# Kernel tuning notes

Measured on AMD Instinct MI355X. Metric: run time of the kernel, lower is better.

The kernel has to match this reference:

```python
import jax, jax.numpy as jnp
import numpy as np

N = 65536      # num ref nodes
M = 65536      # num query nodes
E = 1572864    # num edges (avg degree 24)
K0 = 27        # num kernels (3x3x3 neighborhood)
D1 = 64        # input channels
D2 = 64        # output channels


def setup_inputs() -> dict:
    key = jax.random.key(0)
    k1, k2, k3, k4, k5, k6 = jax.random.split(key, 6)
    # kernel init mirrors initialize_kernel_weight (uniform in [-bound, bound])
    fan_in = D1 * K0
    gain = float(np.sqrt(2.0 / (1.0 + 5.0)))  # leaky_relu gain with slope sqrt(5)
    std = gain / np.sqrt(fan_in)
    bound = float(np.sqrt(3.0) * std)
    kernel = jax.random.uniform(k1, (K0, D1, D2), minval=-bound, maxval=bound, dtype=jnp.float32)
    ref_feat = jax.random.normal(k2, (N, D1), dtype=jnp.float32)
    e_kernel = jax.random.randint(k3, (E,), 0, K0)
    e_ref = jax.random.randint(k4, (E,), 0, N)
    e_query = jax.random.randint(k5, (E,), 0, M)
    e_weight = jax.random.uniform(k6, (E,), dtype=jnp.float32)
    return {
        "kernel": kernel,
        "ref_feat": ref_feat,
        "e_kernel": e_kernel,
        "e_ref": e_ref,
        "e_query": e_query,
        "num_queries": M,
        "e_weight": e_weight,
    }


def reference(kernel, ref_feat, e_kernel, e_ref, e_query, num_queries, e_weight):
    # Math of MessagePassing.forward:
    #   query_feat[m] = sum_{edges e: e_query[e]==m} w_e * (ref_feat[e_ref[e]] @ kernel[e_kernel[e]])
    # Efficient form: precompute each node's transform under every kernel
    # (N*K0*D1*D2 dense GEMM), then gather per edge and scatter-reduce.
    transformed = jnp.einsum('nd,kdo->nko', ref_feat, kernel)   # [N, K0, D2]
    msgs = transformed[e_ref, e_kernel] * e_weight[:, None]      # [E, D2]
    query_feat = jax.ops.segment_sum(msgs, e_query, num_segments=num_queries)  # [M, D2]
    return query_feat
```

## Files before the change

### kernel.cpp

```cpp
#include <hip/hip_runtime.h>

#define DIN 64
#define DOUT 64
#define MAXK 32

typedef __bf16 bf16x8 __attribute__((ext_vector_type(8)));
typedef float  f32x4  __attribute__((ext_vector_type(4)));
typedef unsigned int u32x4 __attribute__((ext_vector_type(4)));

static __device__ inline unsigned short f2b(float x) {
    return __builtin_bit_cast(unsigned short, (__bf16)x);
}
static __device__ inline float b2f(unsigned short u) {
    return __uint_as_float(((unsigned int)u) << 16);
}


__global__ void conv_w_kernel(const float* __restrict__ W,
                              unsigned short* __restrict__ Wt, int total,
                              int* __restrict__ qcount) {
    int i = blockIdx.x * blockDim.x + threadIdx.x;
    if (i < 256) qcount[i] = 0;
    if (i < total) {
        int j    = i & 7;
        int lane = (i >> 3) & 63;
        int h    = (i >> 9) & 1;
        int t    = (i >> 10) & 3;
        int k    = i >> 12;
        int col  = lane & 15;
        int quad = lane >> 4;
        int d1 = h * 32 + quad * 8 + j;
        int d2 = t * 16 + col;
        Wt[i] = f2b(W[(k * 64 + d1) * 64 + d2]);
    }
}


static __device__ __forceinline__ void phaseA_body(
    const float* __restrict__ ref,
    const unsigned short* __restrict__ Wt,
    unsigned short* __restrict__ T,
    int K0, int Nn, int nblk, char* lds)
{
    const int lane = threadIdx.x & 63;
    const int wid  = threadIdx.x >> 6;
    const int col  = lane & 15;
    const int quad = lane >> 4;
    const int n0   = nblk * 64 + wid * 16;
    const int row  = n0 + col;
    char* buf = lds + wid * (16 * 144);

    const float* rp = ref + (size_t)row * 64;
    f32x4 r0 = *reinterpret_cast<const f32x4*>(rp + quad * 8);
    f32x4 r1 = *reinterpret_cast<const f32x4*>(rp + quad * 8 + 4);
    f32x4 r2 = *reinterpret_cast<const f32x4*>(rp + 32 + quad * 8);
    f32x4 r3 = *reinterpret_cast<const f32x4*>(rp + 32 + quad * 8 + 4);
    bf16x8 b0, b1;
    #pragma unroll
    for (int i = 0; i < 4; ++i) {
        b0[i]     = (__bf16)r0[i];
        b0[4 + i] = (__bf16)r1[i];
        b1[i]     = (__bf16)r2[i];
        b1[4 + i] = (__bf16)r3[i];
    }

    const int rrow = lane >> 2;
    const int rq   = lane & 3;

    for (int k = 0; k < K0; ++k) {
        const unsigned short* Wk = Wt + (size_t)k * 4096;
        #pragma unroll
        for (int t = 0; t < 4; ++t) {
            const unsigned short* ap = Wk + (size_t)t * 1024 + lane * 8;
            bf16x8 a0 = *reinterpret_cast<const bf16x8*>(ap);
            bf16x8 a1 = *reinterpret_cast<const bf16x8*>(ap + 512);
            f32x4 c = {0.f, 0.f, 0.f, 0.f};
            c = __builtin_amdgcn_mfma_f32_16x16x32_bf16(a0, b0, c, 0, 0, 0);
            c = __builtin_amdgcn_mfma_f32_16x16x32_bf16(a1, b1, c, 0, 0, 0);
            unsigned int lo = (unsigned int)f2b(c[0]) | ((unsigned int)f2b(c[1]) << 16);
            unsigned int hi = (unsigned int)f2b(c[2]) | ((unsigned int)f2b(c[3]) << 16);
            *reinterpret_cast<uint2*>(buf + col * 144 + t * 32 + quad * 8) =
                make_uint2(lo, hi);
        }
        u32x4 v0 = *reinterpret_cast<const u32x4*>(buf + rrow * 144 + rq * 32);
        u32x4 v1 = *reinterpret_cast<const u32x4*>(buf + rrow * 144 + rq * 32 + 16);
        size_t gbase = ((size_t)k * Nn + n0 + rrow) * 64 + rq * 16;
        *reinterpret_cast<u32x4*>(T + gbase)     = v0;
        *reinterpret_cast<u32x4*>(T + gbase + 8) = v1;
    }
}


__global__ void p1_hist_kernel(const int* __restrict__ eq, int E,
                               int* __restrict__ qcount) {
    __shared__ int l[256];
    l[threadIdx.x] = 0;
    __syncthreads();
    int stride = gridDim.x * blockDim.x;
    for (int i = blockIdx.x * blockDim.x + threadIdx.x; i < E; i += stride)
        atomicAdd(&l[((unsigned)eq[i]) >> 8], 1);
    __syncthreads();
    int v = l[threadIdx.x];
    if (v) atomicAdd(&qcount[threadIdx.x], v);
}

__global__ void p1_scan_kernel(const int* __restrict__ qcount,
                               int* __restrict__ gbase, int* __restrict__ gcursor,
                               int* __restrict__ qstart, int NB, int M, int E) {
    __shared__ int sh[256];
    int t = threadIdx.x;
    int v = (t < NB) ? qcount[t] : 0;
    sh[t] = v;
    __syncthreads();
    #pragma unroll
    for (int o = 1; o < 256; o <<= 1) {
        int x = (t >= o) ? sh[t - o] : 0;
        __syncthreads();
        sh[t] += x;
        __syncthreads();
    }
    int ex = sh[t] - v;
    if (t < NB) { gbase[t] = ex; gcursor[t] = ex; }
    if (t == 0) qstart[M] = E;
}

static __device__ __forceinline__ void scatter_body(
    const int* __restrict__ eq, const int* __restrict__ er,
    const int* __restrict__ ek, const float* __restrict__ ew,
    int E, int* __restrict__ gcursor, uint2* __restrict__ tmp,
    int sblk, int* bin, int* base)
{
    const int t = threadIdx.x;
    bin[t] = 0;
    __syncthreads();
    const int i0 = sblk * 4096;
    unsigned key[16];
    unsigned rank[16];
    uint2 pay[16];
    #pragma unroll
    for (int u = 0; u < 16; ++u) {
        int i = i0 + u * 256 + t;
        if (i < E) {
            int q = eq[i];
            unsigned b = ((unsigned)q) >> 8;
            key[u] = b;
            rank[u] = atomicAdd(&bin[b], 1);
            pay[u] = make_uint2((unsigned)er[i] | ((unsigned)ek[i] << 16) |
                                ((unsigned)(q & 255) << 21),
                                __float_as_uint(ew[i]));
        } else {
            key[u] = 0xFFFFFFFFu;
        }
    }
    __syncthreads();
    int c = bin[t];
    if (c) base[t] = atomicAdd(&gcursor[t], c);
    __syncthreads();
    #pragma unroll
    for (int u = 0; u < 16; ++u) {
        if (key[u] != 0xFFFFFFFFu)
            tmp[(size_t)base[key[u]] + rank[u]] = pay[u];
    }
}

static __device__ __forceinline__ void p2_body(
    const uint2* __restrict__ tmp, const int* __restrict__ gbase,
    const int* __restrict__ qcount, uint2* __restrict__ rec,
    int* __restrict__ qstart, int b, int* fine, int* foff)
{
    const int t = threadIdx.x;
    const int s = gbase[b];
    const int L = qcount[b];
    fine[t] = 0;
    __syncthreads();
    for (int i = t; i < L; i += 256)
        atomicAdd(&fine[(tmp[s + i].x >> 21) & 255], 1);
    __syncthreads();
    int v = fine[t];
    __syncthreads();
    #pragma unroll
    for (int o = 1; o < 256; o <<= 1) {
        int x = (t >= o) ? fine[t - o] : 0;
        __syncthreads();
        fine[t] += x;
        __syncthreads();
    }
    foff[t] = fine[t] - v;
    qstart[b * 256 + t] = s + foff[t];
    __syncthreads();
    fine[t] = 0;
    __syncthreads();
    for (int i = t; i < L; i += 256) {
        uint2 p = tmp[s + i];
        unsigned fb = (p.x >> 21) & 255;
        int r = atomicAdd(&fine[fb], 1);
        rec[(size_t)s + foff[fb] + r] = p;
    }
}


__global__ __launch_bounds__(256) void fusedA_scatter_kernel(
    const float* __restrict__ ref, const unsigned short* __restrict__ Wt,
    unsigned short* __restrict__ T, int K0, int Nn, int NA1,
    const int* __restrict__ eq, const int* __restrict__ er,
    const int* __restrict__ ek, const float* __restrict__ ew,
    int E, int* __restrict__ gcursor, uint2* __restrict__ tmp)
{
    __shared__ __align__(16) char ldsbuf[4 * 16 * 144];
    __shared__ int s0[256];
    __shared__ int s1[256];
    if ((int)blockIdx.x < NA1) {
        phaseA_body(ref, Wt, T, K0, Nn, (int)blockIdx.x, ldsbuf);
    } else {
        scatter_body(eq, er, ek, ew, E, gcursor, tmp,
                     (int)blockIdx.x - NA1, s0, s1);
    }
}

__global__ __launch_bounds__(256) void fusedA_p2_kernel(
    const float* __restrict__ ref, const unsigned short* __restrict__ Wt,
    unsigned short* __restrict__ T, int K0, int Nn, int NA1, int NA2,
    const uint2* __restrict__ tmp, const int* __restrict__ gbase,
    const int* __restrict__ qcount, uint2* __restrict__ rec,
    int* __restrict__ qstart)
{
    __shared__ __align__(16) char ldsbuf[4 * 16 * 144];
    __shared__ int s0[256];
    __shared__ int s1[256];
    if ((int)blockIdx.x < NA2) {
        phaseA_body(ref, Wt, T, K0, Nn, NA1 + (int)blockIdx.x, ldsbuf);
    } else {
        p2_body(tmp, gbase, qcount, rec, qstart,
                (int)blockIdx.x - NA2, s0, s1);
    }
}


__global__ __launch_bounds__(256) void phaseB_kernel(
    const unsigned short* __restrict__ T,
    const uint2* __restrict__ rec,
    const int* __restrict__ qstart,
    float* __restrict__ out, int Nn)
{
    const int lane = threadIdx.x & 63;
    const int wid  = threadIdx.x >> 6;
    const int q    = blockIdx.x * 4 + wid;

    int beg = qstart[q];
    int end = qstart[q + 1];
    int cnt = end - beg;
    float acc = 0.f;

    if (cnt <= 64) {
        uint2 rv = make_uint2(0u, 0u);
        if (lane < cnt) rv = rec[beg + lane];
        int j = 0;
        for (; j + 8 <= cnt; j += 8) {
            float partial[8];
            #pragma unroll
            for (int u = 0; u < 8; ++u) {
                unsigned mx = (unsigned)__builtin_amdgcn_readlane((int)rv.x, j + u);
                unsigned mw = (unsigned)__builtin_amdgcn_readlane((int)rv.y, j + u);
                unsigned off = (((mx >> 16) & 31) * (unsigned)Nn + (mx & 0xFFFFu)) * 64u
                               + (unsigned)lane;
                partial[u] = __uint_as_float(mw) * b2f(T[off]);
            }
            #pragma unroll
            for (int u = 0; u < 8; ++u) acc += partial[u];
        }
        for (; j < cnt; ++j) {
            unsigned mx = (unsigned)__builtin_amdgcn_readlane((int)rv.x, j);
            unsigned mw = (unsigned)__builtin_amdgcn_readlane((int)rv.y, j);
            unsigned off = (((mx >> 16) & 31) * (unsigned)Nn + (mx & 0xFFFFu)) * 64u
                           + (unsigned)lane;
            acc = fmaf(__uint_as_float(mw), b2f(T[off]), acc);
        }
    } else {
        for (int j = beg; j < end; ++j) {
            uint2 v0 = rec[j];
            unsigned m0 = __builtin_amdgcn_readfirstlane(v0.x);
            float w0 = __uint_as_float(__builtin_amdgcn_readfirstlane(v0.y));
            unsigned off = (((m0 >> 16) & 31) * (unsigned)Nn + (m0 & 0xFFFFu)) * 64u
                           + (unsigned)lane;
            acc = fmaf(w0, b2f(T[off]), acc);
        }
    }
    out[(size_t)q * 64 + lane] = acc;
}


__global__ void hist_kernel(const int* __restrict__ ek, int E, int* __restrict__ counts) {
    __shared__ int l[MAXK];
    if (threadIdx.x < MAXK) l[threadIdx.x] = 0;
    __syncthreads();
    int stride = gridDim.x * blockDim.x;
    for (int i = blockIdx.x * blockDim.x + threadIdx.x; i < E; i += stride)
        atomicAdd(&l[ek[i]], 1);
    __syncthreads();
    if (threadIdx.x < MAXK) {
        int v = l[threadIdx.x];
        if (v) atomicAdd(&counts[threadIdx.x], v);
    }
}

__global__ void scan_kernel(const int* __restrict__ counts, int K,
                            int* __restrict__ start, int* __restrict__ cursor) {
    if (threadIdx.x == 0 && blockIdx.x == 0) {
        int acc = 0;
        for (int k = 0; k < K; ++k) {
            start[k] = acc;
            cursor[k] = acc;
            acc += counts[k];
        }
    }
}

__global__ void scatter_kernel(const int* __restrict__ ek, int E,
                               int* __restrict__ cursor, int* __restrict__ sorted) {
    __shared__ int lcnt[MAXK], lbase[MAXK], lpos[MAXK];
    if (threadIdx.x < MAXK) { lcnt[threadIdx.x] = 0; lpos[threadIdx.x] = 0; }
    __syncthreads();
    int i = blockIdx.x * blockDim.x + threadIdx.x;
    int k = 0;
    bool valid = (i < E);
    if (valid) { k = ek[i]; atomicAdd(&lcnt[k], 1); }
    __syncthreads();
    if (threadIdx.x < MAXK) {
        int v = lcnt[threadIdx.x];
        if (v) lbase[threadIdx.x] = atomicAdd(&cursor[threadIdx.x], v);
    }
    __syncthreads();
    if (valid) {
        int slot = lbase[k] + atomicAdd(&lpos[k], 1);
        sorted[slot] = i;
    }
}

__global__ __launch_bounds__(256) void mp_bucket_kernel(
    const float* __restrict__ W, const float* __restrict__ ref,
    const int* __restrict__ e_ref, const int* __restrict__ e_query,
    const float* __restrict__ e_weight, const int* __restrict__ sorted,
    const int* __restrict__ start, const int* __restrict__ counts,
    float* __restrict__ out)
{
    const int k = blockIdx.y;
    const int lane = threadIdx.x & 63;
    const int wid = threadIdx.x >> 6;

    float wreg[DIN];
    const float* Wk = W + k * DIN * DOUT;
    #pragma unroll
    for (int d = 0; d < DIN; ++d) wreg[d] = Wk[d * DOUT + lane];

    const int s = start[k];
    const int c = counts[k];
    const int nwaves = gridDim.x * 4;

    for (int i = blockIdx.x * 4 + wid; i < c; i += nwaves) {
        int eid = __builtin_amdgcn_readfirstlane(sorted[s + i]);
        int r = e_ref[eid];
        int q = e_query[eid];
        float w = e_weight[eid];
        const float* row = ref + r * DIN;
        float a0 = 0.f, a1 = 0.f, a2 = 0.f, a3 = 0.f;
        #pragma unroll
        for (int d = 0; d < DIN; d += 4) {
            a0 += row[d + 0] * wreg[d + 0];
            a1 += row[d + 1] * wreg[d + 1];
            a2 += row[d + 2] * wreg[d + 2];
            a3 += row[d + 3] * wreg[d + 3];
        }
        atomicAdd(&out[q * DOUT + lane], ((a0 + a1) + (a2 + a3)) * w);
    }
}


extern "C" void kernel_launch(void* const* d_in, const int* in_sizes, int n_in,
                              void* d_out, int out_size, void* d_ws, size_t ws_size,
                              hipStream_t stream) {
    const float* W        = (const float*)d_in[0];
    const float* ref      = (const float*)d_in[1];
    const int*   e_kernel = (const int*)d_in[2];
    const int*   e_ref    = (const int*)d_in[3];
    const int*   e_query  = (const int*)d_in[4];
    const float* e_weight = (const float*)d_in[6];

    const int K0 = in_sizes[0] / (DIN * DOUT);
    const int N  = in_sizes[1] / DIN;
    const int E  = in_sizes[2];
    const int M  = out_size / DOUT;
    const int KD = K0 * 64;
    const int NB = M / 256;

    float* out = (float*)d_out;

    size_t off = 0;
    auto alloc = [&](size_t bytes, size_t align) {
        off = (off + align - 1) / align * align;
        size_t r = off; off += bytes; return r;
    };
    size_t o_tmp     = alloc((size_t)E * 8, 16);
    size_t o_rec     = alloc((size_t)E * 8, 16);
    size_t o_qstart  = alloc((size_t)(M + 1) * 4, 4);
    size_t o_qcount  = alloc(256 * 4, 4);
    size_t o_gbase   = alloc(256 * 4, 4);
    size_t o_gcursor = alloc(256 * 4, 4);
    size_t o_wt      = alloc((size_t)K0 * 4096 * 2, 16);
    size_t o_T       = alloc((size_t)N * KD * 2, 16);
    size_t needA = off;

    bool planA_ok = (ws_size >= needA) && (M % 256 == 0) && (NB >= 1) && (NB <= 256) &&
                    (N % 64 == 0) && (N <= 65536) && (K0 <= 32);

    if (planA_ok) {
        char* ws = (char*)d_ws;
        uint2* tmp           = (uint2*)(ws + o_tmp);
        uint2* rec           = (uint2*)(ws + o_rec);
        int*  qstart         = (int*)(ws + o_qstart);
        int*  qcount         = (int*)(ws + o_qcount);
        int*  gbase          = (int*)(ws + o_gbase);
        int*  gcursor        = (int*)(ws + o_gcursor);
        unsigned short* Wt   = (unsigned short*)(ws + o_wt);
        unsigned short* T    = (unsigned short*)(ws + o_T);

        const int NA  = N / 64;
        const int NA1 = (NA + 1) / 2;
        const int NA2 = NA - NA1;
        const int SCB = (E + 4095) / 4096;

        conv_w_kernel<<<(K0 * 4096 + 255) / 256, 256, 0, stream>>>(W, Wt, K0 * 4096,
                                                                   qcount);
        p1_hist_kernel<<<512, 256, 0, stream>>>(e_query, E, qcount);
        p1_scan_kernel<<<1, 256, 0, stream>>>(qcount, gbase, gcursor, qstart, NB, M, E);

        fusedA_scatter_kernel<<<NA1 + SCB, 256, 0, stream>>>(
            ref, Wt, T, K0, N, NA1,
            e_query, e_ref, e_kernel, e_weight, E, gcursor, tmp);

        fusedA_p2_kernel<<<NA2 + NB, 256, 0, stream>>>(
            ref, Wt, T, K0, N, NA1, NA2,
            tmp, gbase, qcount, rec, qstart);

        phaseB_kernel<<<M / 4, 256, 0, stream>>>(T, rec, qstart, out, N);
    } else {
        hipMemsetAsync(out, 0, (size_t)out_size * sizeof(float), stream);
        size_t needB = (size_t)(96 + E) * sizeof(int);
        if (ws_size >= needB) {
            int* ws_i   = (int*)d_ws;
            int* counts = ws_i;
            int* start  = ws_i + 32;
            int* cursor = ws_i + 64;
            int* sorted = ws_i + 96;
            hipMemsetAsync(counts, 0, 96 * sizeof(int), stream);
            hist_kernel<<<512, 256, 0, stream>>>(e_kernel, E, counts);
            scan_kernel<<<1, 64, 0, stream>>>(counts, K0, start, cursor);
            scatter_kernel<<<(E + 255) / 256, 256, 0, stream>>>(e_kernel, E, cursor, sorted);
            dim3 grid(64, K0);
            mp_bucket_kernel<<<grid, 256, 0, stream>>>(W, ref, e_ref, e_query, e_weight,
                                                       sorted, start, counts, out);
        }
    }
}
```

Before: 269.6 us.

## Split phase-A GEMM across four fused launches and prefetch weights in registers

The dense node-by-kernel transform (phase A) is now split into four unevenly sized chunks. Each chunk is co-launched with one of the CSR-build stages (histogram, scan, scatter, fine sort), so the lightweight sort stages overlap with GEMM work instead of running alone. Inside phase A, the next kernel slice's weight fragments are prefetched into registers and the LDS staging buffer is double-buffered by k parity. The larger LDS allocation and extra prefetch registers may reduce occupancy.

After: 276.0 us. +2.4%, slower.

```diff
diff --git a/kernel.cpp b/kernel.cpp
--- a/kernel.cpp
+++ b/kernel.cpp
@@ -36,6 +36,8 @@
 }
 
 
+#define PA_LDS 18432
+
 static __device__ __forceinline__ void phaseA_body(
     const float* __restrict__ ref,
     const unsigned short* __restrict__ Wt,
@@ -48,7 +50,7 @@
     const int quad = lane >> 4;
     const int n0   = nblk * 64 + wid * 16;
     const int row  = n0 + col;
-    char* buf = lds + wid * (16 * 144);
+    char* bufs = lds + wid * 4608;
 
     const float* rp = ref + (size_t)row * 64;
     f32x4 r0 = *reinterpret_cast<const f32x4*>(rp + quad * 8);
@@ -66,48 +68,77 @@
 
     const int rrow = lane >> 2;
     const int rq   = lane & 3;
+    const unsigned short* Wl = Wt + lane * 8;
+
+    bf16x8 c0 = *reinterpret_cast<const bf16x8*>(Wl);
+    bf16x8 c1 = *reinterpret_cast<const bf16x8*>(Wl + 512);
+    bf16x8 c2 = *reinterpret_cast<const bf16x8*>(Wl + 1024);
+    bf16x8 c3 = *reinterpret_cast<const bf16x8*>(Wl + 1536);
+    bf16x8 c4 = *reinterpret_cast<const bf16x8*>(Wl + 2048);
+    bf16x8 c5 = *reinterpret_cast<const bf16x8*>(Wl + 2560);
+    bf16x8 c6 = *reinterpret_cast<const bf16x8*>(Wl + 3072);
+    bf16x8 c7 = *reinterpret_cast<const bf16x8*>(Wl + 3584);
 
     for (int k = 0; k < K0; ++k) {
-        const unsigned short* Wk = Wt + (size_t)k * 4096;
-        #pragma unroll
-        for (int t = 0; t < 4; ++t) {
-            const unsigned short* ap = Wk + (size_t)t * 1024 + lane * 8;
-            bf16x8 a0 = *reinterpret_cast<const bf16x8*>(ap);
-            bf16x8 a1 = *reinterpret_cast<const bf16x8*>(ap + 512);
-            f32x4 c = {0.f, 0.f, 0.f, 0.f};
-            c = __builtin_amdgcn_mfma_f32_16x16x32_bf16(a0, b0, c, 0, 0, 0);
-            c = __builtin_amdgcn_mfma_f32_16x16x32_bf16(a1, b1, c, 0, 0, 0);
-            unsigned int lo = (unsigned int)f2b(c[0]) | ((unsigned int)f2b(c[1]) << 16);
-            unsigned int hi = (unsigned int)f2b(c[2]) | ((unsigned int)f2b(c[3]) << 16);
-            *reinterpret_cast<uint2*>(buf + col * 144 + t * 32 + quad * 8) =
-                make_uint2(lo, hi);
+        bf16x8 p0, p1, p2, p3, p4, p5, p6, p7;
+        if (k + 1 < K0) {
+            const unsigned short* Wn = Wl + (size_t)(k + 1) * 4096;
+            p0 = *reinterpret_cast<const bf16x8*>(Wn);
+            p1 = *reinterpret_cast<const bf16x8*>(Wn + 512);
+            p2 = *reinterpret_cast<const bf16x8*>(Wn + 1024);
+            p3 = *reinterpret_cast<const bf16x8*>(Wn + 1536);
+            p4 = *reinterpret_cast<const bf16x8*>(Wn + 2048);
+            p5 = *reinterpret_cast<const bf16x8*>(Wn + 2560);
+            p6 = *reinterpret_cast<const bf16x8*>(Wn + 3072);
+            p7 = *reinterpret_cast<const bf16x8*>(Wn + 3584);
+        } else {
+            p0 = c0; p1 = c1; p2 = c2; p3 = c3;
+            p4 = c4; p5 = c5; p6 = c6; p7 = c7;
+        }
+        char* buf = bufs + (k & 1) * 2304;
+        {
+            f32x4 a;
+            a = (f32x4){0.f, 0.f, 0.f, 0.f};
+            a = __builtin_amdgcn_mfma_f32_16x16x32_bf16(c0, b0, a, 0, 0, 0);
+            a = __builtin_amdgcn_mfma_f32_16x16x32_bf16(c1, b1, a, 0, 0, 0);
+            *reinterpret_cast<uint2*>(buf + col * 144 + 0 * 32 + quad * 8) =
+                make_uint2((unsigned)f2b(a[0]) | ((unsigned)f2b(a[1]) << 16),
+                           (unsigned)f2b(a[2]) | ((unsigned)f2b(a[3]) << 16));
+            a = (f32x4){0.f, 0.f, 0.f, 0.f};
+            a = __builtin_amdgcn_mfma_f32_16x16x32_bf16(c2, b0, a, 0, 0, 0);
+            a = __builtin_amdgcn_mfma_f32_16x16x32_bf16(c3, b1, a, 0, 0, 0);
+            *reinterpret_cast<uint2*>(buf + col * 144 + 1 * 32 + quad * 8) =
+                make_uint2((unsigned)f2b(a[0]) | ((unsigned)f2b(a[1]) << 16),
+                           (unsigned)f2b(a[2]) | ((unsigned)f2b(a[3]) << 16));
+            a = (f32x4){0.f, 0.f, 0.f, 0.f};
+            a = __builtin_amdgcn_mfma_f32_16x16x32_bf16(c4, b0, a, 0, 0, 0);
+            a = __builtin_amdgcn_mfma_f32_16x16x32_bf16(c5, b1, a, 0, 0, 0);
+            *reinterpret_cast<uint2*>(buf + col * 144 + 2 * 32 + quad * 8) =
+                make_uint2((unsigned)f2b(a[0]) | ((unsigned)f2b(a[1]) << 16),
+                           (unsigned)f2b(a[2]) | ((unsigned)f2b(a[3]) << 16));
+            a = (f32x4){0.f, 0.f, 0.f, 0.f};
+            a = __builtin_amdgcn_mfma_f32_16x16x32_bf16(c6, b0, a, 0, 0, 0);
+            a = __builtin_amdgcn_mfma_f32_16x16x32_bf16(c7, b1, a, 0, 0, 0);
+            *reinterpret_cast<uint2*>(buf + col * 144 + 3 * 32 + quad * 8) =
+                make_uint2((unsigned)f2b(a[0]) | ((unsigned)f2b(a[1]) << 16),
+                           (unsigned)f2b(a[2]) | ((unsigned)f2b(a[3]) << 16));
         }
         u32x4 v0 = *reinterpret_cast<const u32x4*>(buf + rrow * 144 + rq * 32);
         u32x4 v1 = *reinterpret_cast<const u32x4*>(buf + rrow * 144 + rq * 32 + 16);
         size_t gbase = ((size_t)k * Nn + n0 + rrow) * 64 + rq * 16;
         *reinterpret_cast<u32x4*>(T + gbase)     = v0;
         *reinterpret_cast<u32x4*>(T + gbase + 8) = v1;
-    }
-}
-
-
-__global__ void p1_hist_kernel(const int* __restrict__ eq, int E,
-                               int* __restrict__ qcount) {
-    __shared__ int l[256];
-    l[threadIdx.x] = 0;
-    __syncthreads();
-    int stride = gridDim.x * blockDim.x;
-    for (int i = blockIdx.x * blockDim.x + threadIdx.x; i < E; i += stride)
-        atomicAdd(&l[((unsigned)eq[i]) >> 8], 1);
-    __syncthreads();
-    int v = l[threadIdx.x];
-    if (v) atomicAdd(&qcount[threadIdx.x], v);
-}
-
-__global__ void p1_scan_kernel(const int* __restrict__ qcount,
-                               int* __restrict__ gbase, int* __restrict__ gcursor,
-                               int* __restrict__ qstart, int NB, int M, int E) {
-    __shared__ int sh[256];
+        c0 = p0; c1 = p1; c2 = p2; c3 = p3;
+        c4 = p4; c5 = p5; c6 = p6; c7 = p7;
+    }
+}
+
+
+static __device__ __forceinline__ void scan_body(
+    const int* __restrict__ qcount, int* __restrict__ gbase,
+    int* __restrict__ gcursor, int* __restrict__ qstart,
+    int NB, int M, int E, int* sh)
+{
     int t = threadIdx.x;
     int v = (t < NB) ? qcount[t] : 0;
     sh[t] = v;
@@ -199,39 +230,77 @@
 }
 
 
+__global__ __launch_bounds__(256) void fusedA_hist_kernel(
+    const float* __restrict__ ref, const unsigned short* __restrict__ Wt,
+    unsigned short* __restrict__ T, int K0, int Nn, int acnt,
+    const int* __restrict__ eq, int E, int* __restrict__ qcount)
+{
+    __shared__ __align__(16) char ldsbuf[PA_LDS];
+    __shared__ int l[256];
+    if ((int)blockIdx.x < acnt) {
+        phaseA_body(ref, Wt, T, K0, Nn, (int)blockIdx.x, ldsbuf);
+    } else {
+        l[threadIdx.x] = 0;
+        __syncthreads();
+        const int nh = (int)gridDim.x - acnt;
+        const int stride = nh * 256;
+        for (int i = ((int)blockIdx.x - acnt) * 256 + (int)threadIdx.x; i < E;
+             i += stride)
+            atomicAdd(&l[((unsigned)eq[i]) >> 8], 1);
+        __syncthreads();
+        int v = l[threadIdx.x];
+        if (v) atomicAdd(&qcount[threadIdx.x], v);
+    }
+}
+
+__global__ __launch_bounds__(256) void fusedA_scan_kernel(
+    const float* __restrict__ ref, const unsigned short* __restrict__ Wt,
+    unsigned short* __restrict__ T, int K0, int Nn, int aoff, int acnt,
+    const int* __restrict__ qcount, int* __restrict__ gbase,
+    int* __restrict__ gcursor, int* __restrict__ qstart, int NB, int M, int E)
+{
+    __shared__ __align__(16) char ldsbuf[PA_LDS];
+    __shared__ int sh[256];
+    if ((int)blockIdx.x < acnt) {
+        phaseA_body(ref, Wt, T, K0, Nn, aoff + (int)blockIdx.x, ldsbuf);
+    } else {
+        scan_body(qcount, gbase, gcursor, qstart, NB, M, E, sh);
+    }
+}
+
 __global__ __launch_bounds__(256) void fusedA_scatter_kernel(
     const float* __restrict__ ref, const unsigned short* __restrict__ Wt,
-    unsigned short* __restrict__ T, int K0, int Nn, int NA1,
+    unsigned short* __restrict__ T, int K0, int Nn, int aoff, int acnt,
     const int* __restrict__ eq, const int* __restrict__ er,
     const int* __restrict__ ek, const float* __restrict__ ew,
     int E, int* __restrict__ gcursor, uint2* __restrict__ tmp)
 {
-    __shared__ __align__(16) char ldsbuf[4 * 16 * 144];
+    __shared__ __align__(16) char ldsbuf[PA_LDS];
     __shared__ int s0[256];
     __shared__ int s1[256];
-    if ((int)blockIdx.x < NA1) {
-        phaseA_body(ref, Wt, T, K0, Nn, (int)blockIdx.x, ldsbuf);
+    if ((int)blockIdx.x < acnt) {
+        phaseA_body(ref, Wt, T, K0, Nn, aoff + (int)blockIdx.x, ldsbuf);
     } else {
         scatter_body(eq, er, ek, ew, E, gcursor, tmp,
-                     (int)blockIdx.x - NA1, s0, s1);
+                     (int)blockIdx.x - acnt, s0, s1);
     }
 }
 
 __global__ __launch_bounds__(256) void fusedA_p2_kernel(
     const float* __restrict__ ref, const unsigned short* __restrict__ Wt,
-    unsigned short* __restrict__ T, int K0, int Nn, int NA1, int NA2,
+    unsigned short* __restrict__ T, int K0, int Nn, int aoff, int acnt,
     const uint2* __restrict__ tmp, const int* __restrict__ gbase,
     const int* __restrict__ qcount, uint2* __restrict__ rec,
     int* __restrict__ qstart)
 {
-    __shared__ __align__(16) char ldsbuf[4 * 16 * 144];
+    __shared__ __align__(16) char ldsbuf[PA_LDS];
     __shared__ int s0[256];
     __shared__ int s1[256];
-    if ((int)blockIdx.x < NA2) {
-        phaseA_body(ref, Wt, T, K0, Nn, NA1 + (int)blockIdx.x, ldsbuf);
+    if ((int)blockIdx.x < acnt) {
+        phaseA_body(ref, Wt, T, K0, Nn, aoff + (int)blockIdx.x, ldsbuf);
     } else {
         p2_body(tmp, gbase, qcount, rec, qstart,
-                (int)blockIdx.x - NA2, s0, s1);
+                (int)blockIdx.x - acnt, s0, s1);
     }
 }
 
@@ -424,21 +493,28 @@
         unsigned short* T    = (unsigned short*)(ws + o_T);
 
         const int NA  = N / 64;
-        const int NA1 = (NA + 1) / 2;
-        const int NA2 = NA - NA1;
+        const int A1  = (NA * 11) / 32;
+        const int A2  = (NA * 11) / 32;
+        const int A3  = (NA * 5)  / 32;
+        const int A4  = NA - A1 - A2 - A3;
         const int SCB = (E + 4095) / 4096;
 
         conv_w_kernel<<<(K0 * 4096 + 255) / 256, 256, 0, stream>>>(W, Wt, K0 * 4096,
                                                                    qcount);
-        p1_hist_kernel<<<512, 256, 0, stream>>>(e_query, E, qcount);
-        p1_scan_kernel<<<1, 256, 0, stream>>>(qcount, gbase, gcursor, qstart, NB, M, E);
-
-        fusedA_scatter_kernel<<<NA1 + SCB, 256, 0, stream>>>(
-            ref, Wt, T, K0, N, NA1,
+
+        fusedA_hist_kernel<<<A1 + 512, 256, 0, stream>>>(
+            ref, Wt, T, K0, N, A1, e_query, E, qcount);
+
+        fusedA_scan_kernel<<<A2 + 1, 256, 0, stream>>>(
+            ref, Wt, T, K0, N, A1, A2,
+            qcount, gbase, gcursor, qstart, NB, M, E);
+
+        fusedA_scatter_kernel<<<A3 + SCB, 256, 0, stream>>>(
+            ref, Wt, T, K0, N, A1 + A2, A3,
             e_query, e_ref, e_kernel, e_weight, E, gcursor, tmp);
 
-        fusedA_p2_kernel<<<NA2 + NB, 256, 0, stream>>>(
-            ref, Wt, T, K0, N, NA1, NA2,
+        fusedA_p2_kernel<<<A4 + NB, 256, 0, stream>>>(
+            ref, Wt, T, K0, N, A1 + A2 + A3, A4,
             tmp, gbase, qcount, rec, qstart);
 
         phaseB_kernel<<<M / 4, 256, 0, stream>>>(T, rec, qstart, out, N);
```

## Replace two-level bucket sort with per-query CSR and skip unused T rows

Applied to the files above, without the earlier changes.

Replaces the coarse-bin scatter plus fine re-sort with a direct per-query histogram, two-stage scan and atomic-cursor scatter into the final record array, removing the intermediate tmp buffer and one full pass over edges. Adds a (kernel, ref) usage bitmap built during the histogram so later phase-A blocks write only the T rows that some edge gathers. The GEMM work is split across four fused launches in different proportions. This trades global atomics on 65536 counters and bitmap atomicOr traffic for fewer passes, and the edge order within each query is no longer deterministic.

After: 519.5 us. 1.93x slower.

```diff
diff --git a/kernel.cpp b/kernel.cpp
--- a/kernel.cpp
+++ b/kernel.cpp
@@ -18,9 +18,11 @@
 
 __global__ void conv_w_kernel(const float* __restrict__ W,
                               unsigned short* __restrict__ Wt, int total,
-                              int* __restrict__ qcount) {
+                              int* __restrict__ qcount, unsigned* __restrict__ bm,
+                              int M, int KW) {
     int i = blockIdx.x * blockDim.x + threadIdx.x;
-    if (i < 256) qcount[i] = 0;
+    if (i < M) qcount[i] = 0;
+    if (i < KW) bm[i] = 0;
     if (i < total) {
         int j    = i & 7;
         int lane = (i >> 3) & 63;
@@ -39,6 +41,7 @@
 static __device__ __forceinline__ void phaseA_body(
     const float* __restrict__ ref,
     const unsigned short* __restrict__ Wt,
+    const unsigned* __restrict__ bm,
     unsigned short* __restrict__ T,
     int K0, int Nn, int nblk, char* lds)
 {
@@ -66,8 +69,10 @@
 
     const int rrow = lane >> 2;
     const int rq   = lane & 3;
+    const int mybit = (n0 + rrow) & 31;
 
     for (int k = 0; k < K0; ++k) {
+        unsigned bw = bm[((unsigned)(k * Nn + n0)) >> 5];
         const unsigned short* Wk = Wt + (size_t)k * 4096;
         #pragma unroll
         for (int t = 0; t < 4; ++t) {
@@ -84,32 +89,36 @@
         }
         u32x4 v0 = *reinterpret_cast<const u32x4*>(buf + rrow * 144 + rq * 32);
         u32x4 v1 = *reinterpret_cast<const u32x4*>(buf + rrow * 144 + rq * 32 + 16);
-        size_t gbase = ((size_t)k * Nn + n0 + rrow) * 64 + rq * 16;
-        *reinterpret_cast<u32x4*>(T + gbase)     = v0;
-        *reinterpret_cast<u32x4*>(T + gbase + 8) = v1;
-    }
-}
-
-
-__global__ void p1_hist_kernel(const int* __restrict__ eq, int E,
-                               int* __restrict__ qcount) {
-    __shared__ int l[256];
-    l[threadIdx.x] = 0;
-    __syncthreads();
-    int stride = gridDim.x * blockDim.x;
-    for (int i = blockIdx.x * blockDim.x + threadIdx.x; i < E; i += stride)
-        atomicAdd(&l[((unsigned)eq[i]) >> 8], 1);
-    __syncthreads();
-    int v = l[threadIdx.x];
-    if (v) atomicAdd(&qcount[threadIdx.x], v);
-}
-
-__global__ void p1_scan_kernel(const int* __restrict__ qcount,
-                               int* __restrict__ gbase, int* __restrict__ gcursor,
-                               int* __restrict__ qstart, int NB, int M, int E) {
-    __shared__ int sh[256];
-    int t = threadIdx.x;
-    int v = (t < NB) ? qcount[t] : 0;
+        if ((bw >> mybit) & 1u) {
+            size_t gbase = ((size_t)k * Nn + n0 + rrow) * 64 + rq * 16;
+            *reinterpret_cast<u32x4*>(T + gbase)     = v0;
+            *reinterpret_cast<u32x4*>(T + gbase + 8) = v1;
+        }
+    }
+}
+
+
+static __device__ __forceinline__ void hist_body(
+    const int* __restrict__ eq, const int* __restrict__ er,
+    const int* __restrict__ ek, int E, int Nn,
+    int* __restrict__ qcount, unsigned* __restrict__ bm,
+    int sblk, int nsb)
+{
+    const int stride = nsb * 256;
+    for (int i = sblk * 256 + (int)threadIdx.x; i < E; i += stride) {
+        atomicAdd(&qcount[eq[i]], 1);
+        unsigned pos = (unsigned)ek[i] * (unsigned)Nn + (unsigned)er[i];
+        atomicOr(&bm[pos >> 5], 1u << (pos & 31));
+    }
+}
+
+static __device__ __forceinline__ void scan1_body(
+    const int* __restrict__ qcount, int* __restrict__ qstart,
+    int* __restrict__ chunktot, int sb, int* sh)
+{
+    const int t = threadIdx.x;
+    const int idx = sb * 256 + t;
+    int v = qcount[idx];
     sh[t] = v;
     __syncthreads();
     #pragma unroll
@@ -119,121 +128,114 @@
         sh[t] += x;
         __syncthreads();
     }
-    int ex = sh[t] - v;
-    if (t < NB) { gbase[t] = ex; gcursor[t] = ex; }
-    if (t == 0) qstart[M] = E;
+    qstart[idx] = sh[t] - v;
+    if (t == 255) chunktot[sb] = sh[255];
+}
+
+static __device__ __forceinline__ void scan2_body(
+    int* __restrict__ qstart, int* __restrict__ cursor,
+    const int* __restrict__ chunktot, int sb, int M, int E, int* sh)
+{
+    const int t = threadIdx.x;
+    sh[t] = (t < sb) ? chunktot[t] : 0;
+    __syncthreads();
+    #pragma unroll
+    for (int o = 128; o > 0; o >>= 1) {
+        if (t < o) sh[t] += sh[t + o];
+        __syncthreads();
+    }
+    const int base = sh[0];
+    const int idx = sb * 256 + t;
+    int val = qstart[idx] + base;
+    qstart[idx] = val;
+    cursor[idx] = val;
+    if (sb == 0 && t == 0) qstart[M] = E;
 }
 
 static __device__ __forceinline__ void scatter_body(
     const int* __restrict__ eq, const int* __restrict__ er,
     const int* __restrict__ ek, const float* __restrict__ ew,
-    int E, int* __restrict__ gcursor, uint2* __restrict__ tmp,
-    int sblk, int* bin, int* base)
-{
-    const int t = threadIdx.x;
-    bin[t] = 0;
-    __syncthreads();
-    const int i0 = sblk * 4096;
-    unsigned key[16];
-    unsigned rank[16];
-    uint2 pay[16];
-    #pragma unroll
-    for (int u = 0; u < 16; ++u) {
-        int i = i0 + u * 256 + t;
-        if (i < E) {
-            int q = eq[i];
-            unsigned b = ((unsigned)q) >> 8;
-            key[u] = b;
-            rank[u] = atomicAdd(&bin[b], 1);
-            pay[u] = make_uint2((unsigned)er[i] | ((unsigned)ek[i] << 16) |
-                                ((unsigned)(q & 255) << 21),
-                                __float_as_uint(ew[i]));
-        } else {
-            key[u] = 0xFFFFFFFFu;
-        }
-    }
-    __syncthreads();
-    int c = bin[t];
-    if (c) base[t] = atomicAdd(&gcursor[t], c);
-    __syncthreads();
-    #pragma unroll
-    for (int u = 0; u < 16; ++u) {
-        if (key[u] != 0xFFFFFFFFu)
-            tmp[(size_t)base[key[u]] + rank[u]] = pay[u];
-    }
-}
-
-static __device__ __forceinline__ void p2_body(
-    const uint2* __restrict__ tmp, const int* __restrict__ gbase,
-    const int* __restrict__ qcount, uint2* __restrict__ rec,
-    int* __restrict__ qstart, int b, int* fine, int* foff)
-{
-    const int t = threadIdx.x;
-    const int s = gbase[b];
-    const int L = qcount[b];
-    fine[t] = 0;
-    __syncthreads();
-    for (int i = t; i < L; i += 256)
-        atomicAdd(&fine[(tmp[s + i].x >> 21) & 255], 1);
-    __syncthreads();
-    int v = fine[t];
-    __syncthreads();
-    #pragma unroll
-    for (int o = 1; o < 256; o <<= 1) {
-        int x = (t >= o) ? fine[t - o] : 0;
-        __syncthreads();
-        fine[t] += x;
-        __syncthreads();
-    }
-    foff[t] = fine[t] - v;
-    qstart[b * 256 + t] = s + foff[t];
-    __syncthreads();
-    fine[t] = 0;
-    __syncthreads();
-    for (int i = t; i < L; i += 256) {
-        uint2 p = tmp[s + i];
-        unsigned fb = (p.x >> 21) & 255;
-        int r = atomicAdd(&fine[fb], 1);
-        rec[(size_t)s + foff[fb] + r] = p;
-    }
-}
-
+    int E, int* __restrict__ cursor, uint2* __restrict__ rec,
+    int sblk, int nsb)
+{
+    const int stride = nsb * 256;
+    for (int i = sblk * 256 + (int)threadIdx.x; i < E; i += stride) {
+        int q = eq[i];
+        int slot = atomicAdd(&cursor[q], 1);
+        rec[slot] = make_uint2((unsigned)er[i] | ((unsigned)ek[i] << 16),
+                               __float_as_uint(ew[i]));
+    }
+}
+
+
+__global__ __launch_bounds__(256) void fusedA_hist_kernel(
+    const float* __restrict__ ref, const unsigned short* __restrict__ Wt,
+    const unsigned* __restrict__ bm_r, unsigned short* __restrict__ T,
+    int K0, int Nn, int acnt,
+    const int* __restrict__ eq, const int* __restrict__ er,
+    const int* __restrict__ ek, int E,
+    int* __restrict__ qcount, unsigned* __restrict__ bm_w)
+{
+    __shared__ __align__(16) char ldsbuf[4 * 16 * 144];
+    if ((int)blockIdx.x < acnt) {
+        if (bm_r == nullptr) {
+        }
+        phaseA_body(ref, Wt, bm_r, T, K0, Nn, (int)blockIdx.x, ldsbuf);
+    } else {
+        hist_body(eq, er, ek, E, Nn, qcount, bm_w,
+                  (int)blockIdx.x - acnt, (int)gridDim.x - acnt);
+    }
+}
+
+__global__ __launch_bounds__(256) void fusedA_scan1_kernel(
+    const float* __restrict__ ref, const unsigned short* __restrict__ Wt,
+    const unsigned* __restrict__ bm, unsigned short* __restrict__ T,
+    int K0, int Nn, int aoff, int acnt,
+    const int* __restrict__ qcount, int* __restrict__ qstart,
+    int* __restrict__ chunktot)
+{
+    __shared__ __align__(16) char ldsbuf[4 * 16 * 144];
+    __shared__ int sh[256];
+    if ((int)blockIdx.x < acnt) {
+        phaseA_body(ref, Wt, bm, T, K0, Nn, aoff + (int)blockIdx.x, ldsbuf);
+    } else {
+        scan1_body(qcount, qstart, chunktot, (int)blockIdx.x - acnt, sh);
+    }
+}
+
+__global__ __launch_bounds__(256) void fusedA_scan2_kernel(
+    const float* __restrict__ ref, const unsigned short* __restrict__ Wt,
+    const unsigned* __restrict__ bm, unsigned short* __restrict__ T,
+    int K0, int Nn, int aoff, int acnt,
+    int* __restrict__ qstart, int* __restrict__ cursor,
+    const int* __restrict__ chunktot, int M, int E)
+{
+    __shared__ __align__(16) char ldsbuf[4 * 16 * 144];
+    __shared__ int sh[256];
+    if ((int)blockIdx.x < acnt) {
+        phaseA_body(ref, Wt, bm, T, K0, Nn, aoff + (int)blockIdx.x, ldsbuf);
+    } else {
+        scan2_body(qstart, cursor, chunktot, (int)blockIdx.x - acnt, M, E, sh);
+    }
+}
 
 __global__ __launch_bounds__(256) void fusedA_scatter_kernel(
     const float* __restrict__ ref, const unsigned short* __restrict__ Wt,
-    unsigned short* __restrict__ T, int K0, int Nn, int NA1,
+    const unsigned* __restrict__ bm, unsigned short* __restrict__ T,
+    int K0, int Nn, int aoff, int acnt,
     const int* __restrict__ eq, const int* __restrict__ er,
     const int* __restrict__ ek, const float* __restrict__ ew,
-    int E, int* __restrict__ gcursor, uint2* __restrict__ tmp)
+    int E, int* __restrict__ cursor, uint2* __restrict__ rec)
 {
     __shared__ __align__(16) char ldsbuf[4 * 16 * 144];
-    __shared__ int s0[256];
-    __shared__ int s1[256];
-    if ((int)blockIdx.x < NA1) {
-        phaseA_body(ref, Wt, T, K0, Nn, (int)blockIdx.x, ldsbuf);
-    } else {
-        scatter_body(eq, er, ek, ew, E, gcursor, tmp,
-                     (int)blockIdx.x - NA1, s0, s1);
-    }
-}
-
-__global__ __launch_bounds__(256) void fusedA_p2_kernel(
-    const float* __restrict__ ref, const unsigned short* __restrict__ Wt,
-    unsigned short* __restrict__ T, int K0, int Nn, int NA1, int NA2,
-    const uint2* __restrict__ tmp, const int* __restrict__ gbase,
-    const int* __restrict__ qcount, uint2* __restrict__ rec,
-    int* __restrict__ qstart)
-{
-    __shared__ __align__(16) char ldsbuf[4 * 16 * 144];
-    __shared__ int s0[256];
-    __shared__ int s1[256];
-    if ((int)blockIdx.x < NA2) {
-        phaseA_body(ref, Wt, T, K0, Nn, NA1 + (int)blockIdx.x, ldsbuf);
-    } else {
-        p2_body(tmp, gbase, qcount, rec, qstart,
-                (int)blockIdx.x - NA2, s0, s1);
-    }
-}
+    if ((int)blockIdx.x < acnt) {
+        phaseA_body(ref, Wt, bm, T, K0, Nn, aoff + (int)blockIdx.x, ldsbuf);
+    } else {
+        scatter_body(eq, er, ek, ew, E, cursor, rec,
+                     (int)blockIdx.x - acnt, (int)gridDim.x - acnt);
+    }
+}
+
 
 
 __global__ __launch_bounds__(256) void phaseB_kernel(
@@ -374,6 +376,11 @@
     }
 }
 
+__global__ void fill_ones_kernel(unsigned* __restrict__ p, int n) {
+    int i = blockIdx.x * blockDim.x + threadIdx.x;
+    if (i < n) p[i] = 0xFFFFFFFFu;
+}
+
 
 extern "C" void kernel_launch(void* const* d_in, const int* in_sizes, int n_in,
                               void* d_out, int out_size, void* d_ws, size_t ws_size,
@@ -391,6 +398,7 @@
     const int M  = out_size / DOUT;
     const int KD = K0 * 64;
     const int NB = M / 256;
+    const int KW = (K0 * N + 31) / 32;
 
     float* out = (float*)d_out;
 
@@ -399,12 +407,13 @@
         off = (off + align - 1) / align * align;
         size_t r = off; off += bytes; return r;
     };
-    size_t o_tmp     = alloc((size_t)E * 8, 16);
     size_t o_rec     = alloc((size_t)E * 8, 16);
     size_t o_qstart  = alloc((size_t)(M + 1) * 4, 4);
-    size_t o_qcount  = alloc(256 * 4, 4);
-    size_t o_gbase   = alloc(256 * 4, 4);
-    size_t o_gcursor = alloc(256 * 4, 4);
+    size_t o_qcount  = alloc((size_t)M * 4, 4);
+    size_t o_cursor  = alloc((size_t)M * 4, 4);
+    size_t o_chunk   = alloc(256 * 4, 4);
+    size_t o_bitmap  = alloc((size_t)KW * 4, 4);
+    size_t o_ones    = alloc((size_t)KW * 4, 4);
     size_t o_wt      = alloc((size_t)K0 * 4096 * 2, 16);
     size_t o_T       = alloc((size_t)N * KD * 2, 16);
     size_t needA = off;
@@ -414,32 +423,43 @@
 
     if (planA_ok) {
         char* ws = (char*)d_ws;
-        uint2* tmp           = (uint2*)(ws + o_tmp);
         uint2* rec           = (uint2*)(ws + o_rec);
         int*  qstart         = (int*)(ws + o_qstart);
         int*  qcount         = (int*)(ws + o_qcount);
-        int*  gbase          = (int*)(ws + o_gbase);
-        int*  gcursor        = (int*)(ws + o_gcursor);
+        int*  cursor         = (int*)(ws + o_cursor);
+        int*  chunktot       = (int*)(ws + o_chunk);
+        unsigned* bitmap     = (unsigned*)(ws + o_bitmap);
+        unsigned* ones       = (unsigned*)(ws + o_ones);
         unsigned short* Wt   = (unsigned short*)(ws + o_wt);
         unsigned short* T    = (unsigned short*)(ws + o_T);
 
         const int NA  = N / 64;
-        const int NA1 = (NA + 1) / 2;
-        const int NA2 = NA - NA1;
-        const int SCB = (E + 4095) / 4096;
-
-        conv_w_kernel<<<(K0 * 4096 + 255) / 256, 256, 0, stream>>>(W, Wt, K0 * 4096,
-                                                                   qcount);
-        p1_hist_kernel<<<512, 256, 0, stream>>>(e_query, E, qcount);
-        p1_scan_kernel<<<1, 256, 0, stream>>>(qcount, gbase, gcursor, qstart, NB, M, E);
-
-        fusedA_scatter_kernel<<<NA1 + SCB, 256, 0, stream>>>(
-            ref, Wt, T, K0, N, NA1,
-            e_query, e_ref, e_kernel, e_weight, E, gcursor, tmp);
-
-        fusedA_p2_kernel<<<NA2 + NB, 256, 0, stream>>>(
-            ref, Wt, T, K0, N, NA1, NA2,
-            tmp, gbase, qcount, rec, qstart);
+        const int A1  = (NA * 5) / 16;
+        const int A2  = (NA * 3) / 16;
+        const int A3  = (NA * 3) / 16;
+        const int A4  = NA - A1 - A2 - A3;
+
+        int zgrid = (K0 * 4096 > M ? K0 * 4096 : M);
+        if (KW > zgrid) zgrid = KW;
+        conv_w_kernel<<<(zgrid + 255) / 256, 256, 0, stream>>>(
+            W, Wt, K0 * 4096, qcount, bitmap, M, KW);
+        fill_ones_kernel<<<(KW + 255) / 256, 256, 0, stream>>>(ones, KW);
+
+        fusedA_hist_kernel<<<A1 + 512, 256, 0, stream>>>(
+            ref, Wt, ones, T, K0, N, A1,
+            e_query, e_ref, e_kernel, E, qcount, bitmap);
+
+        fusedA_scan1_kernel<<<A2 + NB, 256, 0, stream>>>(
+            ref, Wt, bitmap, T, K0, N, A1, A2,
+            qcount, qstart, chunktot);
+
+        fusedA_scan2_kernel<<<A3 + NB, 256, 0, stream>>>(
+            ref, Wt, bitmap, T, K0, N, A1 + A2, A3,
+            qstart, cursor, chunktot, M, E);
+
+        fusedA_scatter_kernel<<<A4 + 512, 256, 0, stream>>>(
+            ref, Wt, bitmap, T, K0, N, A1 + A2 + A3, A4,
+            e_query, e_ref, e_kernel, e_weight, E, cursor, rec);
 
         phaseB_kernel<<<M / 4, 256, 0, stream>>>(T, rec, qstart, out, N);
     } else {
```
